# Kernel optimization log

Hardware: AMD Instinct MI355X
Metric: run time of the kernel (lower is better)

Reference implementation:

```python
import jax, jax.numpy as jnp
import numpy as np

B, S, D = 2, 2048, 1024
H = 16
DH = D // H
FFN = 4096
EPS = 1e-5
SCALE = 1.0 / np.sqrt(DH).astype(np.float32)


def layer_norm(x, g, b):
    mu = jnp.mean(x, axis=-1, keepdims=True)
    var = jnp.mean(jnp.square(x - mu), axis=-1, keepdims=True)
    return (x - mu) * jax.lax.rsqrt(var + EPS) * g + b


def setup_inputs() -> dict:
    key = jax.random.key(0)
    ks = jax.random.split(key, 12)
    std = 0.02
    return {
        "x": jax.random.normal(ks[0], (B, S, D), dtype=jnp.float32),
        "mask": jax.random.randint(ks[1], (B, S), 0, 2, dtype=jnp.int32),
        "w_qkv": jax.random.normal(ks[2], (D, 3 * D), dtype=jnp.float32) * std,
        "w_out": jax.random.normal(ks[3], (D, D), dtype=jnp.float32) * std,
        "b_out": jnp.zeros((D,), dtype=jnp.float32),
        "g1": jnp.ones((D,), dtype=jnp.float32),
        "be1": jnp.zeros((D,), dtype=jnp.float32),
        "g2": jnp.ones((D,), dtype=jnp.float32),
        "be2": jnp.zeros((D,), dtype=jnp.float32),
        "w1": jax.random.normal(ks[4], (D, FFN), dtype=jnp.float32) * std,
        "b1": jnp.zeros((FFN,), dtype=jnp.float32),
        "w2": jax.random.normal(ks[5], (FFN, D), dtype=jnp.float32) * std,
        "b2": jnp.zeros((D,), dtype=jnp.float32),
    }


def reference(x, mask, w_qkv, w_out, b_out, g1, be1, g2, be2, w1, b1, w2, b2):
    # --- pre-norm self-attention ---
    h = layer_norm(x, g1, be1)                              # [B,S,D]
    qkv = (h @ w_qkv).reshape(B, S, 3, H, DH)               # [B,S,3,H,Dh]
    q, k, v = [jnp.transpose(qkv[:, :, i], (0, 2, 1, 3)) for i in range(3)]  # [B,H,S,Dh]
    scores = jnp.einsum("bhqd,bhkd->bhqk", q, k) * SCALE    # [B,H,S,S]
    key_mask = (mask != 0)[:, None, None, :]                # [B,1,1,S]
    scores = jnp.where(key_mask, scores, -1e9)
    attn = jax.nn.softmax(scores, axis=-1)
    out = jnp.einsum("bhqk,bhkd->bhqd", attn, v)            # [B,H,S,Dh]
    out = jnp.transpose(out, (0, 2, 1, 3)).reshape(B, S, D)
    x = x + (out @ w_out + b_out)
    # --- pre-norm FFN ---
    h2 = layer_norm(x, g2, be2)
    ffn = jax.nn.relu(h2 @ w1 + b1) @ w2 + b2
    return x + ffn
```

## Files before the change

kernel.cpp:

```cpp
#include <hip/hip_runtime.h>

typedef unsigned short u16;
typedef __bf16 bf16x8 __attribute__((ext_vector_type(8)));
typedef float f32x4 __attribute__((ext_vector_type(4)));

typedef __attribute__((address_space(1))) const void* as1cv;
typedef __attribute__((address_space(3))) void* as3v;

__device__ __forceinline__ u16 f2bf(float f) {
  union { float f; unsigned u; } v;
  v.f = f;
  unsigned r = (v.u + 0x7fffu + ((v.u >> 16) & 1u)) >> 16;
  return (u16)r;
}

__device__ __forceinline__ unsigned cvtpk(float lo, float hi) {
  unsigned r;
  asm("v_cvt_pk_bf16_f32 %0, %1, %2" : "=v"(r) : "v"(lo), "v"(hi));
  return r;
}

__device__ __forceinline__ void gload16(const void* g, void* l) {
  __builtin_amdgcn_global_load_lds((as1cv)g, (as3v)l, 16, 0, 0);
}

__global__ __launch_bounds__(256)
void ln_kernel(const float* __restrict__ x, const float* __restrict__ g,
               const float* __restrict__ be, u16* __restrict__ out) {
  __shared__ float red[8];
  const int row = blockIdx.x;
  const int tid = threadIdx.x;
  const float4 v = ((const float4*)(x + (size_t)row * 1024))[tid];
  float s = v.x + v.y + v.z + v.w;
#pragma unroll
  for (int off = 1; off < 64; off <<= 1) s += __shfl_xor(s, off, 64);
  const int wv = tid >> 6, lane = tid & 63;
  if (lane == 0) red[wv] = s;
  __syncthreads();
  s = red[0] + red[1] + red[2] + red[3];
  const float mu = s * (1.0f / 1024.0f);
  const float d0 = v.x - mu, d1 = v.y - mu, d2 = v.z - mu, d3 = v.w - mu;
  float q = d0 * d0 + d1 * d1 + d2 * d2 + d3 * d3;
#pragma unroll
  for (int off = 1; off < 64; off <<= 1) q += __shfl_xor(q, off, 64);
  if (lane == 0) red[4 + wv] = q;
  __syncthreads();
  q = red[4] + red[5] + red[6] + red[7];
  const float inv = rsqrtf(q * (1.0f / 1024.0f) + 1e-5f);
  const float4 gv = ((const float4*)g)[tid];
  const float4 bv = ((const float4*)be)[tid];
  unsigned p0 = (unsigned)f2bf(d0 * inv * gv.x + bv.x) |
                ((unsigned)f2bf(d1 * inv * gv.y + bv.y) << 16);
  unsigned p1 = (unsigned)f2bf(d2 * inv * gv.z + bv.z) |
                ((unsigned)f2bf(d3 * inv * gv.w + bv.w) << 16);
  uint2 o; o.x = p0; o.y = p1;
  *(uint2*)(out + (size_t)row * 1024 + tid * 4) = o;
}

__global__ __launch_bounds__(256)
void transpose_all(const float* __restrict__ i0, u16* __restrict__ o0,
                   const float* __restrict__ i1, u16* __restrict__ o1,
                   const float* __restrict__ i2, u16* __restrict__ o2,
                   const float* __restrict__ i3, u16* __restrict__ o3) {
  __shared__ float t[32][33];
  int id = blockIdx.x;
  const float* in; u16* out; int K, N, nx;
  if (id < 3072)      { in = i0; out = o0; K = 1024; N = 3072; nx = 96; }
  else if (id < 4096) { id -= 3072; in = i1; out = o1; K = 1024; N = 1024; nx = 32; }
  else if (id < 8192) { id -= 4096; in = i2; out = o2; K = 1024; N = 4096; nx = 128; }
  else                { id -= 8192; in = i3; out = o3; K = 4096; N = 1024; nx = 32; }
  const int n0 = (id % nx) * 32, k0 = (id / nx) * 32;
  const int tx = threadIdx.x & 31, ty = threadIdx.x >> 5;
  for (int r = ty; r < 32; r += 8)
    t[r][tx] = in[(size_t)(k0 + r) * N + n0 + tx];
  __syncthreads();
  for (int r = ty; r < 32; r += 8)
    out[(size_t)(n0 + r) * K + k0 + tx] = f2bf(t[tx][r]);
}

__global__ __launch_bounds__(256, 3)
void gemm64(const u16* __restrict__ A, const u16* __restrict__ Bt,
            const float* __restrict__ bias, const float* __restrict__ res,
            float* __restrict__ C, int M, int N, int K) {
  __shared__ u16 As[4][4096];
  __shared__ u16 Bs[4][2048];
  const int tid = threadIdx.x;
  const int wv = tid >> 6, lane = tid & 63;
  const int bm = blockIdx.x * 128;
  const int bn = blockIdx.y * 64;
  const int wr = wv >> 1, wc = wv & 1;
  const int l16 = lane & 15, lh = lane >> 4;

  const int ssk = ((lane & 3) ^ ((lane >> 3) & 3)) << 3;
  const int rdk = (lh ^ ((l16 >> 1) & 3)) << 3;

  f32x4 acc[4][2] = {};

  const u16* Ag = A + (size_t)(bm + wv * 16 + (lane >> 2)) * K + ssk;
  const u16* Bg = Bt + (size_t)(bn + wv * 16 + (lane >> 2)) * K + ssk;

#define STG_A64(buf, ko)  do { \
    gload16(Ag + (ko), &As[buf][wv * 512]); \
    gload16(Ag + (size_t)64 * K + (ko), &As[buf][2048 + wv * 512]); } while (0)
#define STG_B64(buf, ko)  do { \
    gload16(Bg + (ko), &Bs[buf][wv * 512]); } while (0)

  const int nst = K >> 5;
  STG_A64(0, 0); STG_B64(0, 0);
  STG_A64(1, 32); STG_B64(1, 32);
  STG_A64(2, 64); STG_B64(2, 64);

  for (int t = 0; t < nst; ++t) {
    const int cur = t & 3;
    const int rem = nst - t;
    if (rem >= 3)      asm volatile("s_waitcnt vmcnt(6)" ::: "memory");
    else if (rem == 2) asm volatile("s_waitcnt vmcnt(3)" ::: "memory");
    else               asm volatile("s_waitcnt vmcnt(0)" ::: "memory");
    __builtin_amdgcn_s_barrier();
    asm volatile("" ::: "memory");
    const int nxb = (t + 3) & 3;
    bf16x8 af[4], bfv[2];
#pragma unroll
    for (int i = 0; i < 4; i++)
      af[i] = *(const bf16x8*)&As[cur][(wr * 64 + i * 16 + l16) * 32 + rdk];
    bfv[0] = *(const bf16x8*)&Bs[cur][(wc * 32 + l16) * 32 + rdk];
    if (t + 3 < nst) STG_A64(nxb, (t + 3) * 32);
    __builtin_amdgcn_s_setprio(1);
#pragma unroll
    for (int i = 0; i < 4; i++)
      acc[i][0] = __builtin_amdgcn_mfma_f32_16x16x32_bf16(af[i], bfv[0], acc[i][0], 0, 0, 0);
    __builtin_amdgcn_s_setprio(0);
    bfv[1] = *(const bf16x8*)&Bs[cur][(wc * 32 + 16 + l16) * 32 + rdk];
    if (t + 3 < nst) STG_B64(nxb, (t + 3) * 32);
    __builtin_amdgcn_s_setprio(1);
#pragma unroll
    for (int i = 0; i < 4; i++)
      acc[i][1] = __builtin_amdgcn_mfma_f32_16x16x32_bf16(af[i], bfv[1], acc[i][1], 0, 0, 0);
    __builtin_amdgcn_s_setprio(0);
  }
#undef STG_A64
#undef STG_B64

#pragma unroll
  for (int i = 0; i < 4; i++) {
#pragma unroll
    for (int j = 0; j < 2; j++) {
      const int col = bn + wc * 32 + j * 16 + l16;
      const float bv = bias[col];
#pragma unroll
      for (int r = 0; r < 4; r++) {
        const int row = bm + wr * 64 + i * 16 + lh * 4 + r;
        const float v = acc[i][j][r] + bv + res[(size_t)row * N + col];
        C[(size_t)row * N + col] = v;
      }
    }
  }
}

template<int BIAS, int RELU, int MODE>
__global__ __launch_bounds__(512, 2)
void gemm256(const u16* __restrict__ A, const u16* __restrict__ Bt,
             const float* __restrict__ bias, u16* __restrict__ C,
             u16* __restrict__ vt, int M, int N, int K) {
  __shared__ u16 As[2][16384];
  __shared__ u16 Bs[2][16384];
  const int tid = threadIdx.x;
  const int wv = tid >> 6, lane = tid & 63;
  const int l16 = lane & 15, lh = lane >> 4;
  const int wm = wv >> 2, wn = wv & 3;
  const int bm = blockIdx.x * 256, bn = blockIdx.y * 256;

  const int koff = ((lane & 7) ^ ((lane >> 3) & 7)) << 3;
  const int ka0 = ((lh ^ (l16 & 7)) << 3);
  const int ka1 = (((4 + lh) ^ (l16 & 7)) << 3);

  f32x4 acc[8][4] = {};

  const u16* Ag = A + (size_t)(bm + wv * 8 + (lane >> 3)) * K + koff;
  const u16* Bg = Bt + (size_t)(bn + wv * 8 + (lane >> 3)) * K + koff;

#define STAGE256(buf, ko)                                                  \
  do {                                                                     \
    _Pragma("unroll")                                                      \
    for (int j = 0; j < 4; ++j) {                                          \
      gload16(Ag + (size_t)(j * 64) * K + (ko), &As[buf][j * 4096 + wv * 512]); \
      gload16(Bg + (size_t)(j * 64) * K + (ko), &Bs[buf][j * 4096 + wv * 512]); \
    }                                                                      \
  } while (0)

  const int nt = K >> 6;
  STAGE256(0, 0);
  if (nt > 1) STAGE256(1, 64);

  for (int t = 0; t < nt; ++t) {
    const int cur = t & 1;
    if (t + 1 < nt) asm volatile("s_waitcnt vmcnt(8)" ::: "memory");
    else            asm volatile("s_waitcnt vmcnt(0)" ::: "memory");
    __builtin_amdgcn_s_barrier();
    asm volatile("" ::: "memory");
#pragma unroll
    for (int kk = 0; kk < 2; ++kk) {
      const int ko = kk ? ka1 : ka0;
      bf16x8 af[8], bfv[4];
#pragma unroll
      for (int i = 0; i < 8; ++i)
        af[i] = *(const bf16x8*)&As[cur][(wm * 128 + i * 16 + l16) * 64 + ko];
#pragma unroll
      for (int n = 0; n < 4; ++n)
        bfv[n] = *(const bf16x8*)&Bs[cur][(wn * 64 + n * 16 + l16) * 64 + ko];
      __builtin_amdgcn_s_setprio(1);
#pragma unroll
      for (int i = 0; i < 8; ++i)
#pragma unroll
        for (int n = 0; n < 4; ++n)
          acc[i][n] = __builtin_amdgcn_mfma_f32_16x16x32_bf16(af[i], bfv[n], acc[i][n], 0, 0, 0);
      __builtin_amdgcn_s_setprio(0);
    }
    asm volatile("" ::: "memory");
    __builtin_amdgcn_s_barrier();
    asm volatile("" ::: "memory");
    if (t + 2 < nt) STAGE256(cur, (t + 2) * 64);
  }
#undef STAGE256

#pragma unroll
  for (int i = 0; i < 8; ++i)
#pragma unroll
    for (int n = 0; n < 4; ++n) {
      const int col = bn + wn * 64 + n * 16 + l16;
      const float bv = BIAS ? bias[col] : 0.0f;
      if (MODE == 3 && bn >= 2048) {
        const int cc = col - 2048, h = cc >> 6, d = cc & 63;
        const int row0 = bm + wm * 128 + i * 16 + lh * 4;
        const int bb = row0 >> 11, kv0 = row0 & 2047;
        const int p0 = (kv0 & 32) | (((kv0 >> 2) & 3) << 3) | (((kv0 >> 4) & 1) << 2);
        uint2 o;
        o.x = (unsigned)f2bf(acc[i][n][0]) | ((unsigned)f2bf(acc[i][n][1]) << 16);
        o.y = (unsigned)f2bf(acc[i][n][2]) | ((unsigned)f2bf(acc[i][n][3]) << 16);
        *(uint2*)(vt + ((size_t)(bb * 16 + h) * 64 + d) * 2048 + (kv0 & ~63) + p0) = o;
      } else {
#pragma unroll
        for (int r = 0; r < 4; ++r) {
          const int row = bm + wm * 128 + i * 16 + lh * 4 + r;
          float v = acc[i][n][r] + bv;
          if (RELU) v = fmaxf(v, 0.0f);
          C[(size_t)row * N + col] = f2bf(v);
        }
      }
    }
}

__global__ __launch_bounds__(256, 2)
void attn4(const u16* __restrict__ qkv, const u16* __restrict__ vT,
           const int* __restrict__ mask, u16* __restrict__ aout) {
  __shared__ u16 KsS[2][4096];
  __shared__ u16 VsS[2][4096];
  __shared__ float mbL[2048];

  const int tid = threadIdx.x;
  const int wv = tid >> 6, lane = tid & 63;
  const int l16 = lane & 15, lh = lane >> 4;
  const int bh = blockIdx.x, b = bh >> 4, h = bh & 15;
  const int q0 = blockIdx.y * 128 + wv * 32;

  {
    const int4* srcm = (const int4*)(mask + b * 2048);
    float4* dstm = (float4*)mbL;
#pragma unroll
    for (int u = 0; u < 2; ++u) {
      const int4 mv = srcm[tid + u * 256];
      float4 f;
      f.x = mv.x ? 0.f : -1.4426950408889634e9f;
      f.y = mv.y ? 0.f : -1.4426950408889634e9f;
      f.z = mv.z ? 0.f : -1.4426950408889634e9f;
      f.w = mv.w ? 0.f : -1.4426950408889634e9f;
      dstm[tid + u * 256] = f;
    }
  }

  bf16x8 qf[2][2];
#pragma unroll
  for (int qb = 0; qb < 2; ++qb)
#pragma unroll
    for (int c = 0; c < 2; ++c)
      qf[qb][c] = *(const bf16x8*)(qkv + (size_t)(b * 2048 + q0 + qb * 16 + l16) * 3072 + h * 64 + c * 32 + 8 * lh);

  const int rs = (l16 & 7) << 4;
  const int koff0 = ((16 * lh) ^ rs) >> 1;
  const int koff1 = ((64 + 16 * lh) ^ rs) >> 1;
  const int voff0 = koff0, voff1 = koff1;

  const int rl0 = wv * 8 + (lane >> 3);
  const int rl1 = 32 + wv * 8 + (lane >> 3);
  const int glog = (lane & 7) ^ ((lane >> 3) & 7);
  const u16* kg0 = qkv + (size_t)(b * 2048 + rl0) * 3072 + 1024 + h * 64 + 8 * glog;
  const u16* kg1 = qkv + (size_t)(b * 2048 + rl1) * 3072 + 1024 + h * 64 + 8 * glog;
  const u16* vg0 = vT + ((size_t)bh * 64 + rl0) * 2048 + 8 * glog;
  const u16* vg1 = vT + ((size_t)bh * 64 + rl1) * 2048 + 8 * glog;

  gload16(kg0, &KsS[0][wv * 512]);
  gload16(kg1, &KsS[0][2048 + wv * 512]);
  gload16(vg0, &VsS[0][wv * 512]);
  gload16(vg1, &VsS[0][2048 + wv * 512]);
  kg0 += 64 * 3072; kg1 += 64 * 3072; vg0 += 64; vg1 += 64;

  const float CL2 = 0.125f * 1.4426950408889634f;
  f32x4 lsum[2] = {};
  f32x4 oT[4][2] = {};
  union U8 { unsigned u[4]; bf16x8 v; };
  U8 onesu;
  onesu.u[0] = onesu.u[1] = onesu.u[2] = onesu.u[3] = 0x3F803F80u;
  const bf16x8 ones = onesu.v;

  for (int t = 0; t < 32; ++t) {
    asm volatile("s_waitcnt vmcnt(0)" ::: "memory");
    __syncthreads();
    const int cur = t & 1;
    if (t + 1 < 32) {
      const int nx = cur ^ 1;
      gload16(kg0, &KsS[nx][wv * 512]);
      gload16(kg1, &KsS[nx][2048 + wv * 512]);
      gload16(vg0, &VsS[nx][wv * 512]);
      gload16(vg1, &VsS[nx][2048 + wv * 512]);
      kg0 += 64 * 3072; kg1 += 64 * 3072; vg0 += 64; vg1 += 64;
    }

    const u16* Kb = &KsS[cur][0];
    const u16* Vb = &VsS[cur][0];

    f32x4 mbc[4];
#pragma unroll
    for (int n = 0; n < 4; ++n)
      mbc[n] = *(const f32x4*)&mbL[t * 64 + n * 16 + 4 * lh];

    f32x4 s[2][4] = {};
    __builtin_amdgcn_s_setprio(1);
#pragma unroll
    for (int c = 0; c < 2; ++c) {
      const int ko = c ? koff1 : koff0;
      bf16x8 kf[4];
#pragma unroll
      for (int n = 0; n < 4; ++n)
        kf[n] = *(const bf16x8*)(Kb + (n * 16 + l16) * 64 + ko);
#pragma unroll
      for (int qb = 0; qb < 2; ++qb)
#pragma unroll
        for (int n = 0; n < 4; ++n)
          s[qb][n] = __builtin_amdgcn_mfma_f32_16x16x32_bf16(kf[n], qf[qb][c], s[qb][n], 0, 0, 0);
    }
    __builtin_amdgcn_s_setprio(0);

#pragma unroll
    for (int qb = 0; qb < 2; ++qb)
#pragma unroll
      for (int n = 0; n < 4; ++n)
#pragma unroll
        for (int j = 0; j < 4; ++j)
          s[qb][n][j] = __builtin_exp2f(fmaf(s[qb][n][j], CL2, mbc[n][j]));

    U8 pa[2][2];
#pragma unroll
    for (int qb = 0; qb < 2; ++qb)
#pragma unroll
      for (int u = 0; u < 2; ++u) {
        pa[qb][u].u[0] = cvtpk(s[qb][2 * u][0], s[qb][2 * u][1]);
        pa[qb][u].u[1] = cvtpk(s[qb][2 * u][2], s[qb][2 * u][3]);
        pa[qb][u].u[2] = cvtpk(s[qb][2 * u + 1][0], s[qb][2 * u + 1][1]);
        pa[qb][u].u[3] = cvtpk(s[qb][2 * u + 1][2], s[qb][2 * u + 1][3]);
      }

    __builtin_amdgcn_s_setprio(1);
#pragma unroll
    for (int u = 0; u < 2; ++u) {
      const int vo = u ? voff1 : voff0;
      lsum[0] = __builtin_amdgcn_mfma_f32_16x16x32_bf16(ones, pa[0][u].v, lsum[0], 0, 0, 0);
      lsum[1] = __builtin_amdgcn_mfma_f32_16x16x32_bf16(ones, pa[1][u].v, lsum[1], 0, 0, 0);
#pragma unroll
      for (int D = 0; D < 4; ++D) {
        const bf16x8 va = *(const bf16x8*)(Vb + (D * 16 + l16) * 64 + vo);
        oT[D][0] = __builtin_amdgcn_mfma_f32_16x16x32_bf16(va, pa[0][u].v, oT[D][0], 0, 0, 0);
        oT[D][1] = __builtin_amdgcn_mfma_f32_16x16x32_bf16(va, pa[1][u].v, oT[D][1], 0, 0, 0);
      }
    }
    __builtin_amdgcn_s_setprio(0);
  }

#pragma unroll
  for (int qb = 0; qb < 2; ++qb) {
    const float rr = 1.0f / lsum[qb][0];
#pragma unroll
    for (int D = 0; D < 4; ++D) {
      uint2 o;
      o.x = cvtpk(oT[D][qb][0] * rr, oT[D][qb][1] * rr);
      o.y = cvtpk(oT[D][qb][2] * rr, oT[D][qb][3] * rr);
      *(uint2*)(aout + (size_t)(b * 2048 + q0 + qb * 16 + l16) * 1024 + h * 64 + D * 16 + 4 * lh) = o;
    }
  }
}

extern "C" void kernel_launch(void* const* d_in, const int* in_sizes, int n_in,
                              void* d_out, int out_size, void* d_ws, size_t ws_size,
                              hipStream_t stream) {
  (void)in_sizes; (void)n_in; (void)out_size; (void)ws_size;
  const float* x     = (const float*)d_in[0];
  const int*   mask  = (const int*)d_in[1];
  const float* w_qkv = (const float*)d_in[2];
  const float* w_out = (const float*)d_in[3];
  const float* b_out = (const float*)d_in[4];
  const float* g1    = (const float*)d_in[5];
  const float* be1   = (const float*)d_in[6];
  const float* g2    = (const float*)d_in[7];
  const float* be2   = (const float*)d_in[8];
  const float* w1    = (const float*)d_in[9];
  const float* b1    = (const float*)d_in[10];
  const float* w2    = (const float*)d_in[11];
  const float* b2    = (const float*)d_in[12];
  float* out = (float*)d_out;

  char* ws = (char*)d_ws;
  u16* hA    = (u16*)(ws);
  u16* wqkvT = (u16*)(ws + 8388608);
  u16* woutT = (u16*)(ws + 14680064);
  u16* w1T   = (u16*)(ws + 16777216);
  u16* w2T   = (u16*)(ws + 25165824);
  u16* qkv   = (u16*)(ws + 33554432);
  u16* ffn1  = (u16*)(ws + 33554432);
  u16* vTb   = (u16*)(ws + 67108864);
  u16* aout  = (u16*)(ws + 75497472);

  ln_kernel<<<4096, 256, 0, stream>>>(x, g1, be1, hA);
  transpose_all<<<12288, 256, 0, stream>>>(w_qkv, wqkvT, w_out, woutT, w1, w1T, w2, w2T);
  gemm256<0, 0, 3><<<dim3(16, 12), 512, 0, stream>>>(hA, wqkvT, nullptr, qkv, vTb, 4096, 3072, 1024);
  attn4<<<dim3(32, 16), 256, 0, stream>>>(qkv, vTb, mask, aout);
  gemm64<<<dim3(32, 16), 256, 0, stream>>>(aout, woutT, b_out, x, out, 4096, 1024, 1024);
  ln_kernel<<<4096, 256, 0, stream>>>(out, g2, be2, hA);
  gemm256<1, 1, 1><<<dim3(16, 16), 512, 0, stream>>>(hA, w1T, b1, ffn1, nullptr, 4096, 4096, 1024);
  gemm64<<<dim3(32, 16), 256, 0, stream>>>(ffn1, w2T, b2, out, out, 4096, 1024, 4096);
}
```

Measured before the change: 239.9 us.

## Split attention over two KV halves and merge partial outputs in a combine kernel

The attention kernel now splits the 2048-long key/value range into two halves via a third grid dimension. This doubles the number of blocks and raises the occupancy hint from 2 to 4 blocks per CU. Each half writes unnormalized bf16 partial outputs and per-row softmax denominators to scratch space that is reused from already-consumed buffers. A new combine kernel sums the two partials and divides by the total denominator. The aim is better GPU fill and latency hiding, at the cost of an extra kernel launch, extra memory traffic, and rounding the unnormalized partials to bf16.

```diff
diff --git a/kernel.cpp b/kernel.cpp
--- a/kernel.cpp
+++ b/kernel.cpp
@@ -250,9 +250,10 @@
     }
 }
 
-__global__ __launch_bounds__(256, 2)
-void attn4(const u16* __restrict__ qkv, const u16* __restrict__ vT,
-           const int* __restrict__ mask, u16* __restrict__ aout) {
+__global__ __launch_bounds__(256, 4)
+void attn5(const u16* __restrict__ qkv, const u16* __restrict__ vT,
+           const int* __restrict__ mask, u16* __restrict__ oP0,
+           u16* __restrict__ aout, float* __restrict__ lsumP) {
   __shared__ u16 KsS[2][4096];
   __shared__ u16 VsS[2][4096];
   __shared__ float mbL[2048];
@@ -262,6 +263,8 @@
   const int l16 = lane & 15, lh = lane >> 4;
   const int bh = blockIdx.x, b = bh >> 4, h = bh & 15;
   const int q0 = blockIdx.y * 128 + wv * 32;
+  const int z = blockIdx.z;
+  const int kvb = z * 1024;
 
   {
     const int4* srcm = (const int4*)(mask + b * 2048);
@@ -293,10 +296,10 @@
   const int rl0 = wv * 8 + (lane >> 3);
   const int rl1 = 32 + wv * 8 + (lane >> 3);
   const int glog = (lane & 7) ^ ((lane >> 3) & 7);
-  const u16* kg0 = qkv + (size_t)(b * 2048 + rl0) * 3072 + 1024 + h * 64 + 8 * glog;
-  const u16* kg1 = qkv + (size_t)(b * 2048 + rl1) * 3072 + 1024 + h * 64 + 8 * glog;
-  const u16* vg0 = vT + ((size_t)bh * 64 + rl0) * 2048 + 8 * glog;
-  const u16* vg1 = vT + ((size_t)bh * 64 + rl1) * 2048 + 8 * glog;
+  const u16* kg0 = qkv + (size_t)(b * 2048 + kvb + rl0) * 3072 + 1024 + h * 64 + 8 * glog;
+  const u16* kg1 = qkv + (size_t)(b * 2048 + kvb + rl1) * 3072 + 1024 + h * 64 + 8 * glog;
+  const u16* vg0 = vT + ((size_t)bh * 64 + rl0) * 2048 + kvb + 8 * glog;
+  const u16* vg1 = vT + ((size_t)bh * 64 + rl1) * 2048 + kvb + 8 * glog;
 
   gload16(kg0, &KsS[0][wv * 512]);
   gload16(kg1, &KsS[0][2048 + wv * 512]);
@@ -312,11 +315,11 @@
   onesu.u[0] = onesu.u[1] = onesu.u[2] = onesu.u[3] = 0x3F803F80u;
   const bf16x8 ones = onesu.v;
 
-  for (int t = 0; t < 32; ++t) {
+  for (int t = 0; t < 16; ++t) {
     asm volatile("s_waitcnt vmcnt(0)" ::: "memory");
     __syncthreads();
     const int cur = t & 1;
-    if (t + 1 < 32) {
+    if (t + 1 < 16) {
       const int nx = cur ^ 1;
       gload16(kg0, &KsS[nx][wv * 512]);
       gload16(kg1, &KsS[nx][2048 + wv * 512]);
@@ -331,7 +334,7 @@
     f32x4 mbc[4];
 #pragma unroll
     for (int n = 0; n < 4; ++n)
-      mbc[n] = *(const f32x4*)&mbL[t * 64 + n * 16 + 4 * lh];
+      mbc[n] = *(const f32x4*)&mbL[kvb + t * 64 + n * 16 + 4 * lh];
 
     f32x4 s[2][4] = {};
     __builtin_amdgcn_s_setprio(1);
@@ -385,17 +388,48 @@
     __builtin_amdgcn_s_setprio(0);
   }
 
+  u16* dst = z ? aout : oP0;
 #pragma unroll
   for (int qb = 0; qb < 2; ++qb) {
-    const float rr = 1.0f / lsum[qb][0];
+    if (lh == 0)
+      lsumP[(size_t)z * 65536 + (size_t)bh * 2048 + q0 + qb * 16 + l16] = lsum[qb][0];
 #pragma unroll
     for (int D = 0; D < 4; ++D) {
       uint2 o;
-      o.x = cvtpk(oT[D][qb][0] * rr, oT[D][qb][1] * rr);
-      o.y = cvtpk(oT[D][qb][2] * rr, oT[D][qb][3] * rr);
-      *(uint2*)(aout + (size_t)(b * 2048 + q0 + qb * 16 + l16) * 1024 + h * 64 + D * 16 + 4 * lh) = o;
-    }
-  }
+      o.x = cvtpk(oT[D][qb][0], oT[D][qb][1]);
+      o.y = cvtpk(oT[D][qb][2], oT[D][qb][3]);
+      *(uint2*)(dst + (size_t)(b * 2048 + q0 + qb * 16 + l16) * 1024 + h * 64 + D * 16 + 4 * lh) = o;
+    }
+  }
+}
+
+__global__ __launch_bounds__(256)
+void attn_combine(const u16* __restrict__ oP0, const float* __restrict__ lsumP,
+                  u16* __restrict__ aout) {
+  const int m = blockIdx.x;
+  const int b = m >> 11, q = m & 2047;
+  const int col = threadIdx.x * 4;
+  const int h = col >> 6;
+  const size_t bhq = (size_t)(b * 16 + h) * 2048 + q;
+  const float rr = 1.0f / (lsumP[bhq] + lsumP[65536 + bhq]);
+  const size_t idx = (size_t)m * 1024 + col;
+  const uint2 a = *(const uint2*)(oP0 + idx);
+  const uint2 c = *(const uint2*)(aout + idx);
+  union { unsigned u; float f; } t0, t1;
+  float r[4];
+#pragma unroll
+  for (int i = 0; i < 4; ++i) {
+    const unsigned ua = (i < 2) ? a.x : a.y;
+    const unsigned uc = (i < 2) ? c.x : c.y;
+    const int sh = (i & 1) * 16;
+    t0.u = ((ua >> sh) & 0xFFFFu) << 16;
+    t1.u = ((uc >> sh) & 0xFFFFu) << 16;
+    r[i] = (t0.f + t1.f) * rr;
+  }
+  uint2 o;
+  o.x = cvtpk(r[0], r[1]);
+  o.y = cvtpk(r[2], r[3]);
+  *(uint2*)(aout + idx) = o;
 }
 
 extern "C" void kernel_launch(void* const* d_in, const int* in_sizes, int n_in,
@@ -427,11 +461,14 @@
   u16* ffn1  = (u16*)(ws + 33554432);
   u16* vTb   = (u16*)(ws + 67108864);
   u16* aout  = (u16*)(ws + 75497472);
+  u16*   oP0   = (u16*)(ws);
+  float* lsumP = (float*)(ws + 8388608);
 
   ln_kernel<<<4096, 256, 0, stream>>>(x, g1, be1, hA);
   transpose_all<<<12288, 256, 0, stream>>>(w_qkv, wqkvT, w_out, woutT, w1, w1T, w2, w2T);
   gemm256<0, 0, 3><<<dim3(16, 12), 512, 0, stream>>>(hA, wqkvT, nullptr, qkv, vTb, 4096, 3072, 1024);
-  attn4<<<dim3(32, 16), 256, 0, stream>>>(qkv, vTb, mask, aout);
+  attn5<<<dim3(32, 16, 2), 256, 0, stream>>>(qkv, vTb, mask, oP0, aout, lsumP);
+  attn_combine<<<4096, 256, 0, stream>>>(oP0, lsumP, aout);
   gemm64<<<dim3(32, 16), 256, 0, stream>>>(aout, woutT, b_out, x, out, 4096, 1024, 1024);
   ln_kernel<<<4096, 256, 0, stream>>>(out, g2, be2, hA);
   gemm256<1, 1, 1><<<dim3(16, 16), 512, 0, stream>>>(hA, w1T, b1, ffn1, nullptr, 4096, 4096, 1024);
```

New measurement: 317.1 us. 32.2% more time.
